# Kernel optimization log

Hardware: AMD Instinct MI355X
Metric: run time of the kernel (lower is better)

The kernel has to match this reference:

```python
import jax, jax.numpy as jnp
import numpy as np

K = 3
PAD = 1


def _deform_conv(x, offset, weight, bias):
    """torchvision-style deform_conv2d (v1, no mask), stride=1, pad=1, dil=1.
    x: [B,C,H,W], offset: [B,2*K*K,H,W] ordered (dy,dx) per kernel pos (row-major).
    """
    B, C, H, W = x.shape
    K2 = K * K
    off = offset.reshape(B, K2, 2, H, W)
    dy, dx = off[:, :, 0], off[:, :, 1]
    ky = jnp.repeat(jnp.arange(K), K).astype(x.dtype)  # [K2] kernel row offsets
    kx = jnp.tile(jnp.arange(K), K).astype(x.dtype)    # [K2] kernel col offsets
    hh = jnp.arange(H, dtype=x.dtype)
    ww = jnp.arange(W, dtype=x.dtype)
    # sampling positions: [B,K2,H,W]
    py = hh[None, None, :, None] + ky[None, :, None, None] - PAD + dy
    px = ww[None, None, None, :] + kx[None, :, None, None] - PAD + dx
    y0f = jnp.floor(py)
    x0f = jnp.floor(px)
    wy = py - y0f
    wx = px - x0f
    y0 = y0f.astype(jnp.int32)
    x0 = x0f.astype(jnp.int32)
    xf = x.reshape(B, C, H * W)

    def corner(iy, ix, w):
        # zero padding outside the image: contribution masked to 0
        valid = (iy >= 0) & (iy < H) & (ix >= 0) & (ix < W)
        iyc = jnp.clip(iy, 0, H - 1)
        ixc = jnp.clip(ix, 0, W - 1)
        lin = (iyc * W + ixc).reshape(B, -1)                      # [B,K2*H*W]
        g = jnp.take_along_axis(xf, lin[:, None, :], axis=2)     # [B,C,K2*H*W]
        g = g.reshape(B, C, K2, H, W)
        wv = (w * valid.astype(x.dtype))[:, None]                # [B,1,K2,H,W]
        return g * wv

    val = (corner(y0, x0, (1 - wy) * (1 - wx))
           + corner(y0, x0 + 1, (1 - wy) * wx)
           + corner(y0 + 1, x0, wy * (1 - wx))
           + corner(y0 + 1, x0 + 1, wy * wx))                    # [B,C,K2,H,W]
    O = weight.shape[0]
    out = jnp.einsum('ock,bckhw->bohw', weight.reshape(O, C, K2), val)
    return out + bias[None, :, None, None]


def setup_inputs() -> dict:
    key = jax.random.key(0)
    k1, k2, k3, k4, k5 = jax.random.split(key, 5)
    B, C, O, H, W = 4, 64, 64, 128, 128
    fan = C * K * K
    x = jax.random.normal(k1, (B, C, H, W), dtype=jnp.float32)
    w_off = jax.random.normal(k2, (2 * K * K, C, K, K), dtype=jnp.float32) / np.sqrt(fan)
    b_off = jax.random.normal(k3, (2 * K * K,), dtype=jnp.float32) * 0.01
    w_dcn = jax.random.normal(k4, (O, C, K, K), dtype=jnp.float32) / np.sqrt(fan)
    b_dcn = jax.random.normal(k5, (O,), dtype=jnp.float32) * 0.01
    return {"x": x, "w_off": w_off, "b_off": b_off, "w_dcn": w_dcn, "b_dcn": b_dcn}


def reference(x, w_off, b_off, w_dcn, b_dcn):
    offset = jax.lax.conv_general_dilated(
        x, w_off, window_strides=(1, 1), padding=((PAD, PAD), (PAD, PAD)),
        dimension_numbers=('NCHW', 'OIHW', 'NCHW')) + b_off[None, :, None, None]
    return _deform_conv(x, offset, w_dcn, b_dcn)
```

## Files before the change

### kernel.cpp

```cpp
#include <hip/hip_runtime.h>
#include <hip/hip_fp16.h>

#define HH 128
#define WW 128
#define CC 64
#define OO 64
#define HWSZ (HH*WW)

typedef _Float16 f16x8 __attribute__((ext_vector_type(8)));
typedef float    f32x4 __attribute__((ext_vector_type(4)));

__device__ __forceinline__ unsigned short f2h(float f) {
    return __half_as_ushort(__float2half_rn(f));
}

__global__ __launch_bounds__(256) void prep_all(const float* __restrict__ x,
                                                const float* __restrict__ wd,
                                                const float* __restrict__ wo,
                                                unsigned short* __restrict__ xh,
                                                unsigned short* __restrict__ wdtf,
                                                unsigned short* __restrict__ wotf) {
    int t = threadIdx.x;
    if (blockIdx.z == 4) {
        int i = (blockIdx.y * 2 + blockIdx.x) * 256 + t;
        if (i < 36864) {
            int j = i & 7, l = (i >> 3) & 63, nt = (i >> 9) & 3, kcb = i >> 11;
            int k = kcb >> 1, cb = kcb & 1;
            int o = nt * 16 + (l & 15);
            int c = cb * 32 + ((l >> 4) & 3) * 8 + j;
            wdtf[i] = f2h(wd[(o * 64 + c) * 9 + k]);
        } else if (i < 36864 + 18432) {
            int jdx = i - 36864;
            int j = jdx & 7, l = (jdx >> 3) & 63, nt = (jdx >> 9) & 1, kcb = jdx >> 10;
            int k = kcb >> 1, cb = kcb & 1;
            int oc = nt * 16 + (l & 15);
            int c = cb * 32 + ((l >> 4) & 3) * 8 + j;
            wotf[jdx] = f2h(oc < 18 ? wo[(oc * 64 + c) * 9 + k] : 0.0f);
        }
        return;
    }
    __shared__ float tile[64 * 65];
    int w0 = blockIdx.x * 64, h = blockIdx.y, b = blockIdx.z;
    const float* xb = x + ((long)b * CC * HWSZ) + h * WW + w0;
#pragma unroll
    for (int i = 0; i < 16; ++i) {
        int idx = i * 256 + t; int c = idx >> 6, w = idx & 63;
        tile[c * 65 + w] = xb[c * HWSZ + w];
    }
    __syncthreads();
    unsigned short* xo = xh + ((long)((b * HH + h) * WW + w0)) * CC;
#pragma unroll
    for (int i = 0; i < 8; ++i) {
        int idx = i * 256 + t; int w = idx >> 5, c = (idx & 31) * 2;
        ushort2 u;
        u.x = f2h(tile[c * 65 + w]);
        u.y = f2h(tile[(c + 1) * 65 + w]);
        *(ushort2*)(xo + w * CC + c) = u;
    }
}

#define VST 328
#define OST 18

template<int K0, int KN>
__device__ __forceinline__ void sample_seg(const unsigned short* __restrict__ xb,
                                           const float* __restrict__ oprow,
                                           unsigned short* __restrict__ val_s,
                                           int h, int wpx, int spx, int ch8) {
#pragma unroll
    for (int k = K0; k < K0 + KN; ++k) {
        int ky = k / 3, kx = k - ky * 3;
        float2 ov = *(const float2*)(oprow + 2 * k);
        float py  = (float)(h + ky - 1) + ov.x;
        float pxf = (float)(wpx + kx - 1) + ov.y;
        float y0f = floorf(py), x0f = floorf(pxf);
        float wy = py - y0f, wx = pxf - x0f;
        int y0 = (int)y0f, x0 = (int)x0f, y1 = y0 + 1, x1 = x0 + 1;
        bool vy0 = (unsigned)y0 < HH, vy1 = (unsigned)y1 < HH;
        bool vx0 = (unsigned)x0 < WW, vx1 = (unsigned)x1 < WW;
        int y0c = min(max(y0, 0), HH - 1), y1c = min(max(y1, 0), HH - 1);
        int x0c = min(max(x0, 0), WW - 1), x1c = min(max(x1, 0), WW - 1);
        _Float16 h0w = (_Float16)((vy0 && vx0) ? (1.f - wy) * (1.f - wx) : 0.f);
        _Float16 h1w = (_Float16)((vy0 && vx1) ? (1.f - wy) * wx : 0.f);
        _Float16 h2w = (_Float16)((vy1 && vx0) ? wy * (1.f - wx) : 0.f);
        _Float16 h3w = (_Float16)((vy1 && vx1) ? wy * wx : 0.f);
        f16x8 s00 = *(const f16x8*)(xb + (y0c * WW + x0c) * CC + ch8);
        f16x8 s01 = *(const f16x8*)(xb + (y0c * WW + x1c) * CC + ch8);
        f16x8 s10 = *(const f16x8*)(xb + (y1c * WW + x0c) * CC + ch8);
        f16x8 s11 = *(const f16x8*)(xb + (y1c * WW + x1c) * CC + ch8);
        f16x8 a = s00 * h0w + s01 * h1w + s10 * h2w + s11 * h3w;
        *(f16x8*)&val_s[spx * VST + (k - K0) * 64 + ch8] = a;
    }
}

template<int K0, int KN>
__device__ __forceinline__ void mfma_seg(const unsigned short* __restrict__ val_s,
                                         const unsigned short* __restrict__ wdtf,
                                         int m, int q, int wv, int l,
                                         f32x4& acc0, f32x4& acc1) {
#pragma unroll
    for (int ki = 0; ki < KN; ++ki) {
        const unsigned short* vs = &val_s[m * VST + ki * 64 + q * 8];
        f16x8 a00 = *(const f16x8*)(vs);
        f16x8 a01 = *(const f16x8*)(vs + 32);
        f16x8 a10 = *(const f16x8*)(vs + 16 * VST);
        f16x8 a11 = *(const f16x8*)(vs + 16 * VST + 32);
        int kcg = (K0 + ki) * 2;
        f16x8 b0 = *(const f16x8*)(wdtf + (kcg * 4 + wv) * 512 + l * 8);
        f16x8 b1 = *(const f16x8*)(wdtf + ((kcg + 1) * 4 + wv) * 512 + l * 8);
        acc0 = __builtin_amdgcn_mfma_f32_16x16x32_f16(a00, b0, acc0, 0, 0, 0);
        acc1 = __builtin_amdgcn_mfma_f32_16x16x32_f16(a10, b0, acc1, 0, 0, 0);
        acc0 = __builtin_amdgcn_mfma_f32_16x16x32_f16(a01, b1, acc0, 0, 0, 0);
        acc1 = __builtin_amdgcn_mfma_f32_16x16x32_f16(a11, b1, acc1, 0, 0, 0);
    }
}

__global__ __launch_bounds__(256, 4) void fused_dcn(const unsigned short* __restrict__ xh,
                                                    const unsigned short* __restrict__ wotf,
                                                    const float* __restrict__ b_off,
                                                    const unsigned short* __restrict__ wdtf,
                                                    const float* __restrict__ b_dcn,
                                                    float* __restrict__ out) {
    __shared__ __attribute__((aligned(16))) unsigned short shm[3 * 68 * 72];
    __shared__ __attribute__((aligned(16))) float offs[64 * OST];
    unsigned short* xr    = shm;
    unsigned short* val_s = shm;

    int id = blockIdx.x;
    int c8 = id & 7;
    int j  = id >> 3;
    int g  = (j >> 5) * 8 + c8;
    int inner = j & 31;
    int b  = g >> 3;
    int h  = (g & 7) * 16 + (inner >> 1);
    int w0 = (inner & 1) * 64;

    int t = threadIdx.x;
    int l = t & 63, wv = t >> 6;
    int m = l & 15, q = l >> 4;

#pragma unroll
    for (int i = 0; i < 7; ++i) {
        int idx = i * 256 + t;
        if (idx < 1584) {
            int r = idx / 528;
            int rem = idx - r * 528;
            int p = rem >> 3, cc = rem & 7;
            int y = h + r - 1, wx = w0 - 1 + p;
            uint4 v = make_uint4(0u, 0u, 0u, 0u);
            if (((unsigned)y < HH) && ((unsigned)wx < WW))
                v = *(const uint4*)(xh + ((long)((b * HH + y) * WW + wx)) * CC + cc * 8);
            *(uint4*)&xr[(r * 68 + p) * 72 + cc * 8] = v;
        }
    }
    __syncthreads();
    {
        int px0 = wv * 16;
        f32x4 acc0 = {0.f, 0.f, 0.f, 0.f}, acc1 = {0.f, 0.f, 0.f, 0.f};
#pragma unroll
        for (int k = 0; k < 9; ++k) {
            int ky = k / 3, kx = k - ky * 3;
            const unsigned short* ar = &xr[(ky * 68 + px0 + m + kx) * 72 + q * 8];
            f16x8 a0 = *(const f16x8*)(ar);
            f16x8 a1 = *(const f16x8*)(ar + 32);
            const unsigned short* bk = wotf + (k * 2) * 2 * 512 + l * 8;
            f16x8 b00 = *(const f16x8*)(bk);
            f16x8 b01 = *(const f16x8*)(bk + 512);
            f16x8 b10 = *(const f16x8*)(bk + 1024);
            f16x8 b11 = *(const f16x8*)(bk + 1536);
            acc0 = __builtin_amdgcn_mfma_f32_16x16x32_f16(a0, b00, acc0, 0, 0, 0);
            acc0 = __builtin_amdgcn_mfma_f32_16x16x32_f16(a1, b10, acc0, 0, 0, 0);
            acc1 = __builtin_amdgcn_mfma_f32_16x16x32_f16(a0, b01, acc1, 0, 0, 0);
            acc1 = __builtin_amdgcn_mfma_f32_16x16x32_f16(a1, b11, acc1, 0, 0, 0);
        }
        float bo0 = b_off[m];
#pragma unroll
        for (int r = 0; r < 4; ++r)
            offs[(px0 + q * 4 + r) * OST + m] = acc0[r] + bo0;
        if (m < 2) {
            float bo1 = b_off[16 + m];
#pragma unroll
            for (int r = 0; r < 4; ++r)
                offs[(px0 + q * 4 + r) * OST + 16 + m] = acc1[r] + bo1;
        }
    }
    __syncthreads();

    int spx = t >> 3, ch8 = (t & 7) * 8;

    const unsigned short* xb = xh + (long)b * HWSZ * CC;
    int o = wv * 16 + m;
    float bo = b_dcn[o];
    float* outo = out + ((long)(b * OO + o)) * HWSZ + h * WW;

#pragma unroll
    for (int g2 = 0; g2 < 2; ++g2) {
        int wg0 = w0 + g2 * 32;
        const float* oprow = &offs[(g2 * 32 + spx) * OST];
        int wpx = wg0 + spx;

        f32x4 acc0 = {0.f, 0.f, 0.f, 0.f}, acc1 = {0.f, 0.f, 0.f, 0.f};

        sample_seg<0, 5>(xb, oprow, val_s, h, wpx, spx, ch8);
        __syncthreads();
        __builtin_amdgcn_s_setprio(1);
        mfma_seg<0, 5>(val_s, wdtf, m, q, wv, l, acc0, acc1);
        __builtin_amdgcn_s_setprio(0);
        __syncthreads();

        sample_seg<5, 4>(xb, oprow, val_s, h, wpx, spx, ch8);
        __syncthreads();
        __builtin_amdgcn_s_setprio(1);
        mfma_seg<5, 4>(val_s, wdtf, m, q, wv, l, acc0, acc1);
        __builtin_amdgcn_s_setprio(0);

        f32x4 r0 = acc0, r1 = acc1;
        r0[0] += bo; r0[1] += bo; r0[2] += bo; r0[3] += bo;
        r1[0] += bo; r1[1] += bo; r1[2] += bo; r1[3] += bo;
        *(f32x4*)(outo + wg0 + q * 4) = r0;
        *(f32x4*)(outo + wg0 + 16 + q * 4) = r1;
        if (g2 == 0) __syncthreads();
    }
}

extern "C" void kernel_launch(void* const* d_in, const int* in_sizes, int n_in,
                              void* d_out, int out_size, void* d_ws, size_t ws_size,
                              hipStream_t stream) {
    const float* x     = (const float*)d_in[0];
    const float* w_off = (const float*)d_in[1];
    const float* b_off = (const float*)d_in[2];
    const float* w_dcn = (const float*)d_in[3];
    const float* b_dcn = (const float*)d_in[4];
    float* out = (float*)d_out;

    char* ws = (char*)d_ws;
    unsigned short* xh   = (unsigned short*)ws;
    unsigned short* wdtf = (unsigned short*)(ws + 8388608);
    unsigned short* wotf = (unsigned short*)(ws + 8462336);

    hipLaunchKernelGGL(prep_all, dim3(2, 128, 5), dim3(256), 0, stream,
                       x, w_dcn, w_off, xh, wdtf, wotf);
    hipLaunchKernelGGL(fused_dcn, dim3(1024), dim3(256), 0, stream,
                       xh, wotf, b_off, wdtf, b_dcn, out);
}
```

Before: 101.3 us.

## Software-pipeline bilinear sampling with MFMA using double-buffered LDS in 3-tap chunks

Restructures the sampling/GEMM loop into six 3-tap stages with two LDS buffers. Each stage issues the global gathers for the next chunk into registers before running MFMAs on the current buffer, then blends and stores into the other buffer. This hides gather latency behind matrix work and removes one barrier per half. The cost is more live registers (12 f16x8 plus weights), which could cause spills or lower occupancy under launch_bounds(256,4).

```diff
diff --git a/kernel.cpp b/kernel.cpp
--- a/kernel.cpp
+++ b/kernel.cpp
@@ -8,6 +8,7 @@
 #define HWSZ (HH*WW)
 
 typedef _Float16 f16x8 __attribute__((ext_vector_type(8)));
+typedef _Float16 f16x4 __attribute__((ext_vector_type(4)));
 typedef float    f32x4 __attribute__((ext_vector_type(4)));
 
 __device__ __forceinline__ unsigned short f2h(float f) {
@@ -59,16 +60,20 @@
     }
 }
 
-#define VST 328
+#define VST3 200
 #define OST 18
 
-template<int K0, int KN>
-__device__ __forceinline__ void sample_seg(const unsigned short* __restrict__ xb,
-                                           const float* __restrict__ oprow,
-                                           unsigned short* __restrict__ val_s,
-                                           int h, int wpx, int spx, int ch8) {
-#pragma unroll
-    for (int k = K0; k < K0 + KN; ++k) {
+struct Samp { f16x8 s0, s1, s2, s3; f16x4 w; };
+
+template<int G2, int K0>
+__device__ __forceinline__ void issue3(const unsigned short* __restrict__ xb,
+                                       const float* __restrict__ offs,
+                                       int h, int w0, int spx, int ch8, Samp (&S)[3]) {
+    const float* oprow = &offs[(G2 * 32 + spx) * OST];
+    int wpx = w0 + G2 * 32 + spx;
+#pragma unroll
+    for (int ki = 0; ki < 3; ++ki) {
+        int k = K0 + ki;
         int ky = k / 3, kx = k - ky * 3;
         float2 ov = *(const float2*)(oprow + 2 * k);
         float py  = (float)(h + ky - 1) + ov.x;
@@ -80,31 +85,42 @@
         bool vx0 = (unsigned)x0 < WW, vx1 = (unsigned)x1 < WW;
         int y0c = min(max(y0, 0), HH - 1), y1c = min(max(y1, 0), HH - 1);
         int x0c = min(max(x0, 0), WW - 1), x1c = min(max(x1, 0), WW - 1);
-        _Float16 h0w = (_Float16)((vy0 && vx0) ? (1.f - wy) * (1.f - wx) : 0.f);
-        _Float16 h1w = (_Float16)((vy0 && vx1) ? (1.f - wy) * wx : 0.f);
-        _Float16 h2w = (_Float16)((vy1 && vx0) ? wy * (1.f - wx) : 0.f);
-        _Float16 h3w = (_Float16)((vy1 && vx1) ? wy * wx : 0.f);
-        f16x8 s00 = *(const f16x8*)(xb + (y0c * WW + x0c) * CC + ch8);
-        f16x8 s01 = *(const f16x8*)(xb + (y0c * WW + x1c) * CC + ch8);
-        f16x8 s10 = *(const f16x8*)(xb + (y1c * WW + x0c) * CC + ch8);
-        f16x8 s11 = *(const f16x8*)(xb + (y1c * WW + x1c) * CC + ch8);
-        f16x8 a = s00 * h0w + s01 * h1w + s10 * h2w + s11 * h3w;
-        *(f16x8*)&val_s[spx * VST + (k - K0) * 64 + ch8] = a;
-    }
-}
-
-template<int K0, int KN>
-__device__ __forceinline__ void mfma_seg(const unsigned short* __restrict__ val_s,
-                                         const unsigned short* __restrict__ wdtf,
-                                         int m, int q, int wv, int l,
-                                         f32x4& acc0, f32x4& acc1) {
-#pragma unroll
-    for (int ki = 0; ki < KN; ++ki) {
-        const unsigned short* vs = &val_s[m * VST + ki * 64 + q * 8];
+        f16x4 w4;
+        w4[0] = (_Float16)((vy0 && vx0) ? (1.f - wy) * (1.f - wx) : 0.f);
+        w4[1] = (_Float16)((vy0 && vx1) ? (1.f - wy) * wx : 0.f);
+        w4[2] = (_Float16)((vy1 && vx0) ? wy * (1.f - wx) : 0.f);
+        w4[3] = (_Float16)((vy1 && vx1) ? wy * wx : 0.f);
+        S[ki].s0 = *(const f16x8*)(xb + (y0c * WW + x0c) * CC + ch8);
+        S[ki].s1 = *(const f16x8*)(xb + (y0c * WW + x1c) * CC + ch8);
+        S[ki].s2 = *(const f16x8*)(xb + (y1c * WW + x0c) * CC + ch8);
+        S[ki].s3 = *(const f16x8*)(xb + (y1c * WW + x1c) * CC + ch8);
+        S[ki].w = w4;
+    }
+}
+
+__device__ __forceinline__ void finish3(Samp (&S)[3], unsigned short* __restrict__ buf,
+                                        int spx, int ch8) {
+#pragma unroll
+    for (int ki = 0; ki < 3; ++ki) {
+        f16x8 a = S[ki].s0 * S[ki].w[0] + S[ki].s1 * S[ki].w[1]
+                + S[ki].s2 * S[ki].w[2] + S[ki].s3 * S[ki].w[3];
+        *(f16x8*)&buf[spx * VST3 + ki * 64 + ch8] = a;
+    }
+}
+
+template<int K0>
+__device__ __forceinline__ void mfma3(const unsigned short* __restrict__ buf,
+                                      const unsigned short* __restrict__ wdtf,
+                                      int m, int q, int wv, int l,
+                                      f32x4& acc0, f32x4& acc1) {
+    __builtin_amdgcn_s_setprio(1);
+#pragma unroll
+    for (int ki = 0; ki < 3; ++ki) {
+        const unsigned short* vs = &buf[m * VST3 + ki * 64 + q * 8];
         f16x8 a00 = *(const f16x8*)(vs);
         f16x8 a01 = *(const f16x8*)(vs + 32);
-        f16x8 a10 = *(const f16x8*)(vs + 16 * VST);
-        f16x8 a11 = *(const f16x8*)(vs + 16 * VST + 32);
+        f16x8 a10 = *(const f16x8*)(vs + 16 * VST3);
+        f16x8 a11 = *(const f16x8*)(vs + 16 * VST3 + 32);
         int kcg = (K0 + ki) * 2;
         f16x8 b0 = *(const f16x8*)(wdtf + (kcg * 4 + wv) * 512 + l * 8);
         f16x8 b1 = *(const f16x8*)(wdtf + ((kcg + 1) * 4 + wv) * 512 + l * 8);
@@ -113,6 +129,7 @@
         acc0 = __builtin_amdgcn_mfma_f32_16x16x32_f16(a01, b1, acc0, 0, 0, 0);
         acc1 = __builtin_amdgcn_mfma_f32_16x16x32_f16(a11, b1, acc1, 0, 0, 0);
     }
+    __builtin_amdgcn_s_setprio(0);
 }
 
 __global__ __launch_bounds__(256, 4) void fused_dcn(const unsigned short* __restrict__ xh,
@@ -123,8 +140,9 @@
                                                     float* __restrict__ out) {
     __shared__ __attribute__((aligned(16))) unsigned short shm[3 * 68 * 72];
     __shared__ __attribute__((aligned(16))) float offs[64 * OST];
-    unsigned short* xr    = shm;
-    unsigned short* val_s = shm;
+    unsigned short* xr   = shm;
+    unsigned short* bufA = shm;
+    unsigned short* bufB = shm + 32 * VST3;
 
     int id = blockIdx.x;
     int c8 = id & 7;
@@ -193,33 +211,54 @@
     float bo = b_dcn[o];
     float* outo = out + ((long)(b * OO + o)) * HWSZ + h * WW;
 
-#pragma unroll
-    for (int g2 = 0; g2 < 2; ++g2) {
-        int wg0 = w0 + g2 * 32;
-        const float* oprow = &offs[(g2 * 32 + spx) * OST];
-        int wpx = wg0 + spx;
-
-        f32x4 acc0 = {0.f, 0.f, 0.f, 0.f}, acc1 = {0.f, 0.f, 0.f, 0.f};
-
-        sample_seg<0, 5>(xb, oprow, val_s, h, wpx, spx, ch8);
-        __syncthreads();
-        __builtin_amdgcn_s_setprio(1);
-        mfma_seg<0, 5>(val_s, wdtf, m, q, wv, l, acc0, acc1);
-        __builtin_amdgcn_s_setprio(0);
-        __syncthreads();
-
-        sample_seg<5, 4>(xb, oprow, val_s, h, wpx, spx, ch8);
-        __syncthreads();
-        __builtin_amdgcn_s_setprio(1);
-        mfma_seg<5, 4>(val_s, wdtf, m, q, wv, l, acc0, acc1);
-        __builtin_amdgcn_s_setprio(0);
-
+    Samp S[3];
+    f32x4 acc0 = {0.f, 0.f, 0.f, 0.f}, acc1 = {0.f, 0.f, 0.f, 0.f};
+
+    issue3<0, 0>(xb, offs, h, w0, spx, ch8, S);
+    finish3(S, bufA, spx, ch8);
+    __syncthreads();
+
+    issue3<0, 3>(xb, offs, h, w0, spx, ch8, S);
+    mfma3<0>(bufA, wdtf, m, q, wv, l, acc0, acc1);
+    finish3(S, bufB, spx, ch8);
+    __syncthreads();
+
+    issue3<0, 6>(xb, offs, h, w0, spx, ch8, S);
+    mfma3<3>(bufB, wdtf, m, q, wv, l, acc0, acc1);
+    finish3(S, bufA, spx, ch8);
+    __syncthreads();
+
+    issue3<1, 0>(xb, offs, h, w0, spx, ch8, S);
+    mfma3<6>(bufA, wdtf, m, q, wv, l, acc0, acc1);
+    {
         f32x4 r0 = acc0, r1 = acc1;
         r0[0] += bo; r0[1] += bo; r0[2] += bo; r0[3] += bo;
         r1[0] += bo; r1[1] += bo; r1[2] += bo; r1[3] += bo;
-        *(f32x4*)(outo + wg0 + q * 4) = r0;
-        *(f32x4*)(outo + wg0 + 16 + q * 4) = r1;
-        if (g2 == 0) __syncthreads();
+        *(f32x4*)(outo + w0 + q * 4) = r0;
+        *(f32x4*)(outo + w0 + 16 + q * 4) = r1;
+        acc0 = f32x4{0.f, 0.f, 0.f, 0.f};
+        acc1 = f32x4{0.f, 0.f, 0.f, 0.f};
+    }
+    finish3(S, bufB, spx, ch8);
+    __syncthreads();
+
+    issue3<1, 3>(xb, offs, h, w0, spx, ch8, S);
+    mfma3<0>(bufB, wdtf, m, q, wv, l, acc0, acc1);
+    finish3(S, bufA, spx, ch8);
+    __syncthreads();
+
+    issue3<1, 6>(xb, offs, h, w0, spx, ch8, S);
+    mfma3<3>(bufA, wdtf, m, q, wv, l, acc0, acc1);
+    finish3(S, bufB, spx, ch8);
+    __syncthreads();
+
+    mfma3<6>(bufB, wdtf, m, q, wv, l, acc0, acc1);
+    {
+        f32x4 r0 = acc0, r1 = acc1;
+        r0[0] += bo; r0[1] += bo; r0[2] += bo; r0[3] += bo;
+        r1[0] += bo; r1[1] += bo; r1[2] += bo; r1[3] += bo;
+        *(f32x4*)(outo + w0 + 32 + q * 4) = r0;
+        *(f32x4*)(outo + w0 + 48 + q * 4) = r1;
     }
 }
 
```

Measured after the change: 103.0 us. About the same (+1.7%).
